# Performance work log

Hardware: AMD Instinct MI355X
Metric: run time of the kernel (lower is better)

Reference implementation:

```python
import jax, jax.numpy as jnp
import numpy as np

B, C_I, C_O, K, H, W = 8, 64, 64, 3, 256, 256
GROUPS = 16  # int(c_o / min(4, c_o)) = 64/4
EPS = 1e-5
PAD = K  # pad_x = pad_y = k + (bc-1) with bc_x=bc_y=1, k=3


def _conv(x, w):
    # x: (B, C_i, h, w), w: (C_o, C_i, K, K), valid conv, stride 1
    return jax.lax.conv_general_dilated(
        x, w, window_strides=(1, 1), padding='VALID',
        dimension_numbers=('NCHW', 'OIHW', 'NCHW'))


def setup_inputs() -> dict:
    key = jax.random.key(0)
    ks = jax.random.split(key, 10)
    s = 1.0 / np.sqrt(C_I * K * K)  # torch Conv2d default init bound
    wshape = (C_O, C_I, K, K)
    names = ['w_int', 'w_tl', 'w_tr', 'w_bl', 'w_br', 'w_top', 'w_bot', 'w_left', 'w_right']
    d = {'x': jax.random.normal(ks[0], (B, C_I, H, W), dtype=jnp.float32)}
    for i, n in enumerate(names):
        d[n] = jax.random.uniform(ks[i + 1], wshape, jnp.float32, -s, s)
    d['bias'] = jnp.zeros((1, C_O, 1, 1), jnp.float32)   # learnable_bias (init zeros)
    d['gamma'] = jnp.ones((C_O,), jnp.float32)           # GroupNorm weight
    d['beta'] = jnp.zeros((C_O,), jnp.float32)           # GroupNorm bias
    return d


def reference(x, w_int, w_tl, w_tr, w_bl, w_br, w_top, w_bot, w_left, w_right, bias, gamma, beta):
    p = PAD
    # corners -> (B,C,1,1)
    tl = _conv(x[:, :, :p, :p], w_tl)
    tr = _conv(x[:, :, :p, -p:], w_tr)
    bl = _conv(x[:, :, -p:, :p], w_bl)
    br = _conv(x[:, :, -p:, -p:], w_br)
    # edges -> (B,C,1,W-2) / (B,C,H-2,1)
    top = _conv(x[:, :, :p, :], w_top)
    bot = _conv(x[:, :, -p:, :], w_bot)
    left = _conv(x[:, :, :, :p], w_left)
    right = _conv(x[:, :, :, -p:], w_right)
    # interior -> (B,C,H-2,W-2)
    mid = _conv(x, w_int)
    mid = jnp.concatenate([left, mid, right], axis=3)       # (B,C,H-2,W)
    top_row = jnp.concatenate([tl, top, tr], axis=3)        # (B,C,1,W)
    bot_row = jnp.concatenate([bl, bot, br], axis=3)        # (B,C,1,W)
    # NOTE: original code puts the 'bottom' conv output first along dim 2
    y = jnp.concatenate([bot_row, mid, top_row], axis=2) + bias  # (B,C,H,W)
    # GroupNorm(16, 64)
    yg = y.reshape(B, GROUPS, -1)
    mu = jnp.mean(yg, axis=2, keepdims=True)
    var = jnp.var(yg, axis=2, keepdims=True)
    yn = ((yg - mu) * jax.lax.rsqrt(var + EPS)).reshape(B, C_O, H, W)
    yn = yn * gamma[None, :, None, None] + beta[None, :, None, None]
    # SELU activation; dropout(rate=0) is identity
    return jax.nn.selu(yn)
```

## Files before the change

kernel.cpp:

```cpp
#include <hip/hip_runtime.h>

#define B_ 8
#define CI 64
#define CO 64
#define H_ 256
#define W_ 256
#define EPS_ 1e-5f

#define SELU_SCALE 1.0507009873554805f
#define SELU_SA    1.7580993408473766f

typedef __attribute__((ext_vector_type(8))) short short8;
typedef __attribute__((ext_vector_type(4))) float f32x4;
typedef unsigned int u32;

__device__ __forceinline__ unsigned short f2bf(float f) {
    unsigned int u = __float_as_uint(f);
    u = (u + 0x7fffu + ((u >> 16) & 1u)) >> 16;
    return (unsigned short)u;
}
__device__ __forceinline__ float bf2f(unsigned short h) {
    return __uint_as_float(((unsigned)h) << 16);
}
__device__ __forceinline__ float selu_f(float u) {
    return (u > 0.f) ? SELU_SCALE * u : SELU_SA * (__expf(u) - 1.f);
}
__device__ __forceinline__ void gload_lds16(const void* g, void* l) {
    __builtin_amdgcn_global_load_lds(
        (const __attribute__((address_space(1))) u32*)g,
        (__attribute__((address_space(3))) u32*)l, 16, 0, 0);
}

__global__ __launch_bounds__(256) void prepass_fused(
    const float* __restrict__ x,
    const float* __restrict__ w_int,
    const float* __restrict__ w_bl, const float* __restrict__ w_br,
    const float* __restrict__ w_tl, const float* __restrict__ w_tr,
    const float* __restrict__ w_bot, const float* __restrict__ w_top,
    const float* __restrict__ w_left, const float* __restrict__ w_right,
    unsigned short* __restrict__ xpre,
    unsigned short* __restrict__ wpre9, float* __restrict__ wedge)
{
    __shared__ unsigned short ls[256 * 72];
    const int blk = blockIdx.x, t = threadIdx.x;

    if (blk < 2048) {
        const int row = blk & 255, b = blk >> 8;
        const int colq = t >> 2;
        const float* xb = x + ((size_t)(b * 64) * 256 + row) * 256;

        for (int sp = 0; sp < 4; ++sp) {
            const int cibase = sp * 16 + (t & 3) * 4;
            float4 v[4];
#pragma unroll
            for (int e = 0; e < 4; ++e)
                v[e] = *(const float4*)(xb + (size_t)(cibase + e) * 65536 + colq * 4);
#pragma unroll
            for (int jj = 0; jj < 4; ++jj) {
                const int col = colq * 4 + jj;
                const int sw  = (col & 7) << 3;
                ushort4 pk;
                pk.x = f2bf((&v[0].x)[jj]);
                pk.y = f2bf((&v[1].x)[jj]);
                pk.z = f2bf((&v[2].x)[jj]);
                pk.w = f2bf((&v[3].x)[jj]);
                *(ushort4*)&ls[col * 72 + (cibase ^ sw)] = pk;
            }
        }
        __syncthreads();
        unsigned short* xp = xpre + ((size_t)(b * 256 + row)) * 256 * 64;
        for (int q = 0; q < 8; ++q) {
            const int lin = q * 256 + t;
            const int col = lin >> 3, k = lin & 7;
            *(uint4*)(xp + col * 64 + k * 8) = *(const uint4*)&ls[col * 72 + k * 8];
        }
    } else {
        const int wb = blk - 2048;
        const int wid = wb / 9, pos = wb % 9;
        const float* src = (wid == 0) ? w_bl : (wid == 1) ? w_br
                         : (wid == 2) ? w_tl : (wid == 3) ? w_tr
                         : (wid == 4) ? w_bot : (wid == 5) ? w_top
                         : (wid == 6) ? w_left : (wid == 7) ? w_right : w_int;
        for (int k = 0; k < 16; ++k) {
            const int lin = k * 256 + t;
            const int co = lin >> 6, cip = lin & 63;
            const int ci = cip ^ ((co & 7) << 3);
            wpre9[(size_t)wid * 36864 + pos * 4096 + lin] =
                f2bf(src[(co * 64 + ci) * 9 + pos]);
            if (wid < 8) {
                const int c4 = lin >> 8, co2 = (lin >> 2) & 63, j = lin & 3;
                const int ci2 = c4 * 4 + j;
                wedge[(size_t)wid * 36864 + pos * 4096 + lin] =
                    src[(co2 * 64 + ci2) * 9 + pos];
            }
        }
    }
}

__global__ __launch_bounds__(512, 4) void conv_all(
    const unsigned short* __restrict__ xpre, const unsigned short* __restrict__ wpre9,
    const float* __restrict__ wedge, const float* __restrict__ bias,
    unsigned short* __restrict__ ybf, float* __restrict__ part)
{
    __shared__ unsigned short xs[10 * 40 * 64];
    __shared__ unsigned short wl3[3][4096];
    __shared__ float sred[8][16][2];
    const int t = threadIdx.x, w = t >> 6, lane = t & 63;
    const int b = blockIdx.z;
    const int l15 = lane & 15, lg = lane >> 4;
    const int sw15 = (l15 & 7) << 3;

    if (blockIdx.y < 32) {
        const unsigned short* wpre = wpre9 + 8 * 36864;
        const int r0 = blockIdx.y * 8, c0 = blockIdx.x * 32;

        for (int L = w; L < 50; L += 8) {
            const int j = L / 5, i = L % 5;
            int rr = r0 - 1 + j; rr = rr < 0 ? 0 : (rr > 255 ? 255 : rr);
            int col = c0 - 2 + i * 8 + (lane >> 3);
            col = col < 0 ? 0 : (col > 255 ? 255 : col);
            gload_lds16((const char*)xpre +
                            ((size_t)((b * 256 + rr) * 256 + col)) * 128 + (lane & 7) * 16,
                        (char*)xs + j * 5120 + i * 1024);
        }
        gload_lds16((const char*)wpre + 0 * 8192 + w * 1024 + lane * 16,
                    (char*)wl3[0] + w * 1024);
        gload_lds16((const char*)wpre + 1 * 8192 + w * 1024 + lane * 16,
                    (char*)wl3[1] + w * 1024);

        int jb[3];
#pragma unroll
        for (int kr = 0; kr < 3; ++kr) jb[kr] = (w + kr) * 5120;
        int offb[3][2][2];
#pragma unroll
        for (int kc = 0; kc < 3; ++kc)
#pragma unroll
            for (int n = 0; n < 2; ++n) {
                const int s = n * 16 + l15 + kc + 1;
#pragma unroll
                for (int ks = 0; ks < 2; ++ks) {
                    const int cib = ks * 32 + lg * 8;
                    offb[kc][n][ks] = s * 128 + ((cib ^ (((s + 6) & 7) << 3)) << 1);
                }
            }
        int afo[2][4];
#pragma unroll
        for (int ks = 0; ks < 2; ++ks)
#pragma unroll
            for (int m = 0; m < 4; ++m) {
                const int cib = ks * 32 + lg * 8;
                afo[ks][m] = (m * 16 + l15) * 128 + ((cib ^ sw15) << 1);
            }

        f32x4 acc[4][2];
#pragma unroll
        for (int m = 0; m < 4; ++m)
#pragma unroll
            for (int n = 0; n < 2; ++n)
                acc[m][n] = (f32x4){0.f, 0.f, 0.f, 0.f};

#pragma unroll
        for (int pos = 0; pos < 9; ++pos) {
            if (pos < 8) asm volatile("s_waitcnt vmcnt(1)" ::: "memory");
            else         asm volatile("s_waitcnt vmcnt(0)" ::: "memory");
            __builtin_amdgcn_s_barrier();
            __builtin_amdgcn_sched_barrier(0);
            if (pos + 2 <= 8)
                gload_lds16((const char*)wpre + (pos + 2) * 8192 + w * 1024 + lane * 16,
                            (char*)wl3[(pos + 2) % 3] + w * 1024);
            const int kr = pos / 3, kc = pos % 3;
            const char* wbuf = (const char*)wl3[pos % 3];
#pragma unroll
            for (int ks = 0; ks < 2; ++ks) {
                short8 bf[2], af[4];
#pragma unroll
                for (int n = 0; n < 2; ++n)
                    bf[n] = *(const short8*)((const char*)xs + jb[kr] + offb[kc][n][ks]);
#pragma unroll
                for (int m = 0; m < 4; ++m)
                    af[m] = *(const short8*)(wbuf + afo[ks][m]);
                __builtin_amdgcn_s_setprio(1);
#pragma unroll
                for (int m = 0; m < 4; ++m)
#pragma unroll
                    for (int n = 0; n < 2; ++n)
                        acc[m][n] = __builtin_amdgcn_mfma_f32_16x16x32_bf16(
                            af[m], bf[n], acc[m][n], 0, 0, 0);
                __builtin_amdgcn_s_setprio(0);
            }
        }

        const int r = r0 + w;
        const bool rmask = (r != 0) && (r != 255);
        float s4[4] = {0.f, 0.f, 0.f, 0.f}, q4[4] = {0.f, 0.f, 0.f, 0.f};
#pragma unroll
        for (int m = 0; m < 4; ++m)
#pragma unroll
            for (int n = 0; n < 2; ++n) {
                const int c = c0 + n * 16 + l15;
                const bool pmask = rmask && (c != 0) && (c != 255);
#pragma unroll
                for (int reg = 0; reg < 4; ++reg) {
                    const int co = m * 16 + lg * 4 + reg;
                    const float v = acc[m][n][reg] + bias[co];
                    if (pmask) {
                        ybf[(((size_t)b * 64 + co) * 256 + r) * 256 + c] = f2bf(v);
                        s4[m] += v; q4[m] += v * v;
                    }
                }
            }
#pragma unroll
        for (int off = 1; off < 16; off <<= 1)
#pragma unroll
            for (int m = 0; m < 4; ++m) {
                s4[m] += __shfl_xor(s4[m], off);
                q4[m] += __shfl_xor(q4[m], off);
            }
        if (l15 == 0) {
#pragma unroll
            for (int m = 0; m < 4; ++m) {
                sred[w][m * 4 + lg][0] = s4[m];
                sred[w][m * 4 + lg][1] = q4[m];
            }
        }
        __syncthreads();
        if (t < 32) {
            const int g = t & 15, sel = t >> 4;
            float v = 0.f;
#pragma unroll
            for (int ww = 0; ww < 8; ++ww) v += sred[ww][g][sel];
            const int slot = blockIdx.y * 8 + blockIdx.x;
            part[((size_t)(b * 512 + slot) * 16 + g) * 2 + sel] = v;
        }
        return;
    }

    const int job = (blockIdx.y - 32) * 8 + blockIdx.x;
    if (job > 24) return;

    if (job < 16) {
        const int edge = job >> 3, seg = job & 7;
        const int c0 = seg * 32;
        const char* wsrc = (const char*)wpre9 + (size_t)(4 + edge) * 73728;
        for (int L = w; L < 15; L += 8) {
            const int j = L / 5, i = L % 5;
            const int rr = (edge == 0) ? (253 + j) : j;
            int col = c0 - 2 + i * 8 + (lane >> 3);
            col = col < 0 ? 0 : (col > 255 ? 255 : col);
            gload_lds16((const char*)xpre +
                            ((size_t)((b * 256 + rr) * 256 + col)) * 128 + (lane & 7) * 16,
                        (char*)xs + j * 5120 + i * 1024);
        }
        gload_lds16(wsrc + 0 * 8192 + w * 1024 + lane * 16, (char*)wl3[0] + w * 1024);
        gload_lds16(wsrc + 1 * 8192 + w * 1024 + lane * 16, (char*)wl3[1] + w * 1024);

        const int cot = w & 3, nh = w >> 2;
        int offb2[3][2];
#pragma unroll
        for (int kc = 0; kc < 3; ++kc) {
            const int s = nh * 16 + l15 + kc + 1;
#pragma unroll
            for (int ks = 0; ks < 2; ++ks) {
                const int cib = ks * 32 + lg * 8;
                offb2[kc][ks] = s * 128 + ((cib ^ (((s + 6) & 7) << 3)) << 1);
            }
        }
        int afo2[2];
#pragma unroll
        for (int ks = 0; ks < 2; ++ks) {
            const int cib = ks * 32 + lg * 8;
            afo2[ks] = (cot * 16 + l15) * 128 + ((cib ^ sw15) << 1);
        }
        f32x4 acc0 = (f32x4){0.f, 0.f, 0.f, 0.f};

#pragma unroll
        for (int pos = 0; pos < 9; ++pos) {
            if (pos < 8) asm volatile("s_waitcnt vmcnt(1)" ::: "memory");
            else         asm volatile("s_waitcnt vmcnt(0)" ::: "memory");
            __builtin_amdgcn_s_barrier();
            __builtin_amdgcn_sched_barrier(0);
            if (pos + 2 <= 8)
                gload_lds16(wsrc + (pos + 2) * 8192 + w * 1024 + lane * 16,
                            (char*)wl3[(pos + 2) % 3] + w * 1024);
            const int kr = pos / 3, kc = pos % 3;
            const char* wbuf = (const char*)wl3[pos % 3];
#pragma unroll
            for (int ks = 0; ks < 2; ++ks) {
                const short8 bf = *(const short8*)((const char*)xs + kr * 5120 + offb2[kc][ks]);
                const short8 af = *(const short8*)(wbuf + afo2[ks]);
                acc0 = __builtin_amdgcn_mfma_f32_16x16x32_bf16(af, bf, acc0, 0, 0, 0);
            }
        }

        const int r_out = edge ? 255 : 0;
        const int c = c0 + nh * 16 + l15;
        const bool pmask = (c != 0) && (c != 255);
        float s = 0.f, q = 0.f;
#pragma unroll
        for (int reg = 0; reg < 4; ++reg) {
            const int co = cot * 16 + lg * 4 + reg;
            const float v = acc0[reg] + bias[co];
            if (pmask) {
                ybf[(((size_t)b * 64 + co) * 256 + r_out) * 256 + c] = f2bf(v);
                s += v; q += v * v;
            }
        }
        s += __shfl_xor(s, 1); q += __shfl_xor(q, 1);
        s += __shfl_xor(s, 2); q += __shfl_xor(q, 2);
        s += __shfl_xor(s, 4); q += __shfl_xor(q, 4);
        s += __shfl_xor(s, 8); q += __shfl_xor(q, 8);
        float* sb = (float*)sred;
        if (l15 == 0) { sb[(w * 4 + lg) * 2] = s; sb[(w * 4 + lg) * 2 + 1] = q; }
        __syncthreads();
        if (t < 32) {
            const int g = t & 15, sel = t >> 4;
            const int ct = g >> 2, sub = g & 3;
            const float v = sb[(ct * 4 + sub) * 2 + sel] + sb[((ct + 4) * 4 + sub) * 2 + sel];
            part[((size_t)(b * 512 + 256 + job) * 16 + g) * 2 + sel] = v;
        }
    } else if (job < 24) {
        const int jj = job - 16;
        const int edge = jj >> 2, seg = jj & 3;
        const int r0 = seg * 64;
        const int colbase = edge ? 253 : 0;
        unsigned short* xr = xs;
        for (int u = t; u < 1584; u += 512) {
            const int row = u / 24, rem = u % 24;
            const int cl = rem >> 3, sub = rem & 7;
            int rr = r0 - 1 + row; rr = rr < 0 ? 0 : (rr > 255 ? 255 : rr);
            const int col = colbase + cl;
            const uint4 v = *(const uint4*)(xpre +
                ((size_t)((b * 256 + rr) * 256 + col)) * 64 + sub * 8);
            *(uint4*)((char*)xr + row * 400 + cl * 128 + sub * 16) = v;
        }
        const char* wsrc = (const char*)wpre9 + (size_t)(6 + edge) * 73728;
        gload_lds16(wsrc + 0 * 8192 + w * 1024 + lane * 16, (char*)wl3[0] + w * 1024);
        gload_lds16(wsrc + 1 * 8192 + w * 1024 + lane * 16, (char*)wl3[1] + w * 1024);
        asm volatile("s_waitcnt lgkmcnt(0)" ::: "memory");

        const int cot = w & 3, np = w >> 2;
        int offlr[3][2];
#pragma unroll
        for (int kc = 0; kc < 3; ++kc) {
            const int key = (colbase + kc) & 7;
#pragma unroll
            for (int ks = 0; ks < 2; ++ks) {
                const int cib = ks * 32 + lg * 8;
                offlr[kc][ks] = kc * 128 + ((cib ^ (key << 3)) << 1);
            }
        }
        int rowb2[2];
#pragma unroll
        for (int j = 0; j < 2; ++j) rowb2[j] = ((np * 2 + j) * 16 + l15) * 400;
        int afo2[2];
#pragma unroll
        for (int ks = 0; ks < 2; ++ks) {
            const int cib = ks * 32 + lg * 8;
            afo2[ks] = (cot * 16 + l15) * 128 + ((cib ^ sw15) << 1);
        }
        f32x4 accA = (f32x4){0.f, 0.f, 0.f, 0.f};
        f32x4 accB = (f32x4){0.f, 0.f, 0.f, 0.f};

#pragma unroll
        for (int pos = 0; pos < 9; ++pos) {
            if (pos < 8) asm volatile("s_waitcnt vmcnt(1)" ::: "memory");
            else         asm volatile("s_waitcnt vmcnt(0)" ::: "memory");
            __builtin_amdgcn_s_barrier();
            __builtin_amdgcn_sched_barrier(0);
            if (pos + 2 <= 8)
                gload_lds16(wsrc + (pos + 2) * 8192 + w * 1024 + lane * 16,
                            (char*)wl3[(pos + 2) % 3] + w * 1024);
            const int kr = pos / 3, kc = pos % 3;
            const char* wbuf = (const char*)wl3[pos % 3];
#pragma unroll
            for (int ks = 0; ks < 2; ++ks) {
                const short8 af = *(const short8*)(wbuf + afo2[ks]);
                const short8 bfA = *(const short8*)((const char*)xr + rowb2[0] + kr * 400 + offlr[kc][ks]);
                const short8 bfB = *(const short8*)((const char*)xr + rowb2[1] + kr * 400 + offlr[kc][ks]);
                accA = __builtin_amdgcn_mfma_f32_16x16x32_bf16(af, bfA, accA, 0, 0, 0);
                accB = __builtin_amdgcn_mfma_f32_16x16x32_bf16(af, bfB, accB, 0, 0, 0);
            }
        }

        const int c_out = edge ? 255 : 0;
        float s = 0.f, q = 0.f;
#pragma unroll
        for (int j = 0; j < 2; ++j) {
            const int r = r0 + (np * 2 + j) * 16 + l15;
            const bool pmask = (r != 0) && (r != 255);
            const f32x4 a = j ? accB : accA;
#pragma unroll
            for (int reg = 0; reg < 4; ++reg) {
                const int co = cot * 16 + lg * 4 + reg;
                const float v = a[reg] + bias[co];
                if (pmask) {
                    ybf[(((size_t)b * 64 + co) * 256 + r) * 256 + c_out] = f2bf(v);
                    s += v; q += v * v;
                }
            }
        }
        s += __shfl_xor(s, 1); q += __shfl_xor(q, 1);
        s += __shfl_xor(s, 2); q += __shfl_xor(q, 2);
        s += __shfl_xor(s, 4); q += __shfl_xor(q, 4);
        s += __shfl_xor(s, 8); q += __shfl_xor(q, 8);
        float* sb = (float*)sred;
        if (l15 == 0) { sb[(w * 4 + lg) * 2] = s; sb[(w * 4 + lg) * 2 + 1] = q; }
        __syncthreads();
        if (t < 32) {
            const int g = t & 15, sel = t >> 4;
            const int ct = g >> 2, sub = g & 3;
            const float v = sb[(ct * 4 + sub) * 2 + sel] + sb[((ct + 4) * 4 + sub) * 2 + sel];
            part[((size_t)(b * 512 + 272 + jj) * 16 + g) * 2 + sel] = v;
        }
    } else {
        float* cred = (float*)sred;
        if (w < 4) {
            const int corner = w, co = lane;
            const int row0 = (corner < 2) ? 253 : 0;
            const int col0 = (corner & 1) ? 253 : 0;
            const int r_out = (corner < 2) ? 0 : 255;
            const int c_out = (corner & 1) ? 255 : 0;
            const float* wbase = wedge + (size_t)corner * 36864;
            float a0 = 0.f, a1 = 0.f, a2 = 0.f, a3 = 0.f;
#pragma unroll 1
            for (int pos = 0; pos < 9; ++pos) {
                const int kr = pos / 3, kc = pos % 3;
                const int row = row0 + kr, col = col0 + kc;
                const unsigned short* xp = xpre + ((size_t)((b * 256 + row) * 256 + col)) * 64;
                const int sw = (col & 7) << 3;
#pragma unroll
                for (int c4 = 0; c4 < 16; ++c4) {
                    const float4 wv = *(const float4*)(wbase + pos * 4096 + c4 * 256 + co * 4);
                    const ushort4 xv = *(const ushort4*)(xp + ((c4 * 4) ^ sw));
                    a0 = fmaf(wv.x, bf2f(xv.x), a0);
                    a1 = fmaf(wv.y, bf2f(xv.y), a1);
                    a2 = fmaf(wv.z, bf2f(xv.z), a2);
                    a3 = fmaf(wv.w, bf2f(xv.w), a3);
                }
            }
            const float v = (a0 + a1) + (a2 + a3) + bias[co];
            ybf[(((size_t)b * 64 + co) * 256 + r_out) * 256 + c_out] = f2bf(v);
            float s = v, q = v * v;
            s += __shfl_xor(s, 1); q += __shfl_xor(q, 1);
            s += __shfl_xor(s, 2); q += __shfl_xor(q, 2);
            if ((co & 3) == 0) {
                cred[(corner * 16 + (co >> 2)) * 2]     = s;
                cred[(corner * 16 + (co >> 2)) * 2 + 1] = q;
            }
        }
        __syncthreads();
        if (t < 32) {
            const int g = t & 15, sel = t >> 4;
            const float r = cred[(0 * 16 + g) * 2 + sel] + cred[(1 * 16 + g) * 2 + sel] +
                            cred[(2 * 16 + g) * 2 + sel] + cred[(3 * 16 + g) * 2 + sel];
            part[((size_t)(b * 512 + 280) * 16 + g) * 2 + sel] = r;
        }
    }
}

__global__ __launch_bounds__(256) void norm_bf2(
    const unsigned short* __restrict__ ybf, float* __restrict__ out,
    const float* __restrict__ part,
    const float* __restrict__ gamma, const float* __restrict__ beta)
{
    __shared__ float wred[4][2];
    __shared__ float mvs[2];
    const int t = threadIdx.x;
    const size_t e0 = (size_t)blockIdx.x * 2048;
    const int b  = (int)(e0 >> 22);
    const int ch = (int)((e0 >> 16) & 63);
    const int g  = ch >> 2;

    float s = 0.f, q = 0.f;
    for (int slot = t; slot < 281; slot += 256) {
        const size_t base = ((size_t)(b * 512 + slot) * 16 + g) * 2;
        s += part[base]; q += part[base + 1];
    }
#pragma unroll
    for (int off = 32; off; off >>= 1) {
        s += __shfl_down(s, off);
        q += __shfl_down(q, off);
    }
    if ((t & 63) == 0) { wred[t >> 6][0] = s; wred[t >> 6][1] = q; }
    __syncthreads();
    if (t == 0) {
        const float S = wred[0][0] + wred[1][0] + wred[2][0] + wred[3][0];
        const float Q = wred[0][1] + wred[1][1] + wred[2][1] + wred[3][1];
        const float inv_n = 1.0f / (4.0f * 65536.0f);
        const float mean = S * inv_n;
        const float var  = Q * inv_n - mean * mean;
        mvs[0] = mean;
        mvs[1] = rsqrtf(var + EPS_);
    }
    __syncthreads();
    const float mean = mvs[0], rstd = mvs[1];
    const float ga = gamma[ch] * rstd;
    const float be = beta[ch] - mean * ga;

    const size_t e = e0 + (size_t)t * 8;
    const uint4 v = *(const uint4*)(ybf + e);
    float f[8];
    f[0] = __uint_as_float(v.x << 16); f[1] = __uint_as_float(v.x & 0xffff0000u);
    f[2] = __uint_as_float(v.y << 16); f[3] = __uint_as_float(v.y & 0xffff0000u);
    f[4] = __uint_as_float(v.z << 16); f[5] = __uint_as_float(v.z & 0xffff0000u);
    f[6] = __uint_as_float(v.w << 16); f[7] = __uint_as_float(v.w & 0xffff0000u);
    float4 o0, o1;
    o0.x = selu_f(f[0] * ga + be); o0.y = selu_f(f[1] * ga + be);
    o0.z = selu_f(f[2] * ga + be); o0.w = selu_f(f[3] * ga + be);
    o1.x = selu_f(f[4] * ga + be); o1.y = selu_f(f[5] * ga + be);
    o1.z = selu_f(f[6] * ga + be); o1.w = selu_f(f[7] * ga + be);
    *(float4*)(out + e)     = o0;
    *(float4*)(out + e + 4) = o1;
}

__global__ __launch_bounds__(256) void conv_main(
    const float* __restrict__ x, const float* __restrict__ w,
    const float* __restrict__ bias, float* __restrict__ y)
{
    const int c = threadIdx.x;
    const int r = blockIdx.x;
    const int b = blockIdx.y;
    const int rr = (r == 0) ? (H_ - 3) : ((r == H_ - 1) ? 0 : (r - 1));
    const int cc = min(max(c - 1, 0), W_ - 3);
    float acc[CO];
#pragma unroll
    for (int co = 0; co < CO; ++co) acc[co] = 0.f;
    const float* xb = x + (size_t)b * CI * H_ * W_;
    for (int ci = 0; ci < CI; ++ci) {
        const float* xp = xb + ((size_t)ci * H_ + rr) * W_ + cc;
        float xv[9];
#pragma unroll
        for (int kr = 0; kr < 3; ++kr)
#pragma unroll
            for (int kc = 0; kc < 3; ++kc)
                xv[kr * 3 + kc] = xp[kr * W_ + kc];
        const float* wci = w + ci * 9;
#pragma unroll
        for (int co = 0; co < CO; ++co) {
            const float* wp = wci + co * (CI * 9);
            float a = acc[co];
#pragma unroll
            for (int k = 0; k < 9; ++k) a = fmaf(xv[k], wp[k], a);
            acc[co] = a;
        }
    }
#pragma unroll
    for (int co = 0; co < CO; ++co)
        y[(((size_t)b * CO + co) * H_ + r) * W_ + c] = acc[co] + bias[co];
}

__global__ __launch_bounds__(256) void conv_edge(
    const float* __restrict__ x,
    const float* __restrict__ w_bot, const float* __restrict__ w_top,
    const float* __restrict__ w_left, const float* __restrict__ w_right,
    const float* __restrict__ bias, float* __restrict__ y)
{
    const int b     = blockIdx.x;
    const int edge  = blockIdx.y;
    const int seg   = blockIdx.z;
    const int el    = threadIdx.x & 63;
    const int chunk = threadIdx.x >> 6;
    const int e     = seg * 64 + el;
    const bool active = (e < 254);
    const int ec    = active ? e : 253;
    const float* w = (edge == 0) ? w_bot : (edge == 1) ? w_top
                   : (edge == 2) ? w_left : w_right;
    int r_out, c_out, rr, cc;
    if (edge == 0)      { r_out = 0;      c_out = 1 + ec; rr = H_ - 3; cc = ec; }
    else if (edge == 1) { r_out = H_ - 1; c_out = 1 + ec; rr = 0;      cc = ec; }
    else if (edge == 2) { r_out = 1 + ec; c_out = 0;      rr = ec;     cc = 0; }
    else                { r_out = 1 + ec; c_out = W_ - 1; rr = ec;     cc = W_ - 3; }
    float acc[CO];
#pragma unroll
    for (int co = 0; co < CO; ++co) acc[co] = 0.f;
    const float* xb = x + (size_t)b * CI * H_ * W_;
    const int ci0 = chunk * 16;
    for (int ci = ci0; ci < ci0 + 16; ++ci) {
        const float* xp = xb + ((size_t)ci * H_ + rr) * W_ + cc;
        float xv[9];
#pragma unroll
        for (int kr = 0; kr < 3; ++kr)
#pragma unroll
            for (int kc = 0; kc < 3; ++kc)
                xv[kr * 3 + kc] = xp[kr * W_ + kc];
#pragma unroll
        for (int co = 0; co < CO; ++co) {
            const float* wp = w + co * (CI * 9) + ci * 9;
            float a = acc[co];
#pragma unroll
            for (int k = 0; k < 9; ++k) a = fmaf(xv[k], wp[k], a);
            acc[co] = a;
        }
    }
    __shared__ float lds[64][65];
    for (int s = 0; s < 4; ++s) {
        if (chunk == s) {
            if (s == 0) {
#pragma unroll
                for (int co = 0; co < CO; ++co) lds[el][co] = acc[co];
            } else {
#pragma unroll
                for (int co = 0; co < CO; ++co) lds[el][co] += acc[co];
            }
        }
        __syncthreads();
    }
    if (chunk == 0 && active) {
#pragma unroll
        for (int co = 0; co < CO; ++co)
            y[(((size_t)b * CO + co) * H_ + r_out) * W_ + c_out] = lds[el][co] + bias[co];
    }
}

__global__ __launch_bounds__(256) void conv_corner(
    const float* __restrict__ x,
    const float* __restrict__ w_bl, const float* __restrict__ w_br,
    const float* __restrict__ w_tl, const float* __restrict__ w_tr,
    const float* __restrict__ bias, float* __restrict__ y)
{
    const int b      = blockIdx.x;
    const int corner = threadIdx.x >> 6;
    const int co     = threadIdx.x & 63;
    const float* w = (corner == 0) ? w_bl : (corner == 1) ? w_br
                   : (corner == 2) ? w_tl : w_tr;
    const int rr    = (corner < 2) ? (H_ - 3) : 0;
    const int cc    = (corner & 1) ? (W_ - 3) : 0;
    const int r_out = (corner < 2) ? 0 : (H_ - 1);
    const int c_out = (corner & 1) ? (W_ - 1) : 0;
    const float* xb = x + (size_t)b * CI * H_ * W_;
    float a = 0.f;
    for (int ci = 0; ci < CI; ++ci) {
        const float* xp = xb + ((size_t)ci * H_ + rr) * W_ + cc;
        const float* wp = w + ((size_t)co * CI + ci) * 9;
#pragma unroll
        for (int kr = 0; kr < 3; ++kr)
#pragma unroll
            for (int kc = 0; kc < 3; ++kc)
                a = fmaf(xp[kr * W_ + kc], wp[kr * 3 + kc], a);
    }
    y[(((size_t)b * CO + co) * H_ + r_out) * W_ + c_out] = a + bias[co];
}

__global__ __launch_bounds__(256) void stats_kernel(
    const float* __restrict__ y, float* __restrict__ ws)
{
    const int bid   = blockIdx.x;
    const int chunk = bid & 3;
    const int g     = (bid >> 2) & 15;
    const int b     = bid >> 6;
    const float* p  = y + ((size_t)(b * 64 + g * 4 + chunk)) * (H_ * W_);
    float s = 0.f, q = 0.f;
    for (int i = threadIdx.x; i < (H_ * W_ / 4); i += 256) {
        float4 v = reinterpret_cast<const float4*>(p)[i];
        s += v.x + v.y + v.z + v.w;
        q += v.x * v.x + v.y * v.y + v.z * v.z + v.w * v.w;
    }
#pragma unroll
    for (int off = 32; off; off >>= 1) {
        s += __shfl_down(s, off);
        q += __shfl_down(q, off);
    }
    __shared__ float red[8];
    const int wid = threadIdx.x >> 6;
    if ((threadIdx.x & 63) == 0) { red[wid * 2] = s; red[wid * 2 + 1] = q; }
    __syncthreads();
    if (threadIdx.x == 0) {
        ws[bid * 2]     = red[0] + red[2] + red[4] + red[6];
        ws[bid * 2 + 1] = red[1] + red[3] + red[5] + red[7];
    }
}

__global__ __launch_bounds__(256) void norm_stats(
    float* __restrict__ y, const float* __restrict__ st,
    const float* __restrict__ gamma, const float* __restrict__ beta)
{
    const size_t t = (size_t)blockIdx.x * 256 + threadIdx.x;
    const size_t e = t * 4;
    const int b  = (int)(e >> 22);
    const int ch = (int)((e >> 16) & 63);
    const int g  = ch >> 2;
    const int sb = ((b * 16 + g) * 4) * 2;
    const float S = st[sb] + st[sb + 2] + st[sb + 4] + st[sb + 6];
    const float Q = st[sb + 1] + st[sb + 3] + st[sb + 5] + st[sb + 7];
    const float inv_n = 1.0f / (4.0f * H_ * W_);
    const float mean  = S * inv_n;
    const float var   = Q * inv_n - mean * mean;
    const float rstd  = rsqrtf(var + EPS_);
    const float ga = gamma[ch] * rstd;
    const float be = beta[ch] - mean * ga;
    float4 v = reinterpret_cast<float4*>(y)[t];
    float u;
    u = v.x * ga + be; v.x = selu_f(u);
    u = v.y * ga + be; v.y = selu_f(u);
    u = v.z * ga + be; v.z = selu_f(u);
    u = v.w * ga + be; v.w = selu_f(u);
    reinterpret_cast<float4*>(y)[t] = v;
}

extern "C" void kernel_launch(void* const* d_in, const int* in_sizes, int n_in,
                              void* d_out, int out_size, void* d_ws, size_t ws_size,
                              hipStream_t stream) {
    const float* x       = (const float*)d_in[0];
    const float* w_int   = (const float*)d_in[1];
    const float* w_tl    = (const float*)d_in[2];
    const float* w_tr    = (const float*)d_in[3];
    const float* w_bl    = (const float*)d_in[4];
    const float* w_br    = (const float*)d_in[5];
    const float* w_top   = (const float*)d_in[6];
    const float* w_bot   = (const float*)d_in[7];
    const float* w_left  = (const float*)d_in[8];
    const float* w_right = (const float*)d_in[9];
    const float* bias    = (const float*)d_in[10];
    const float* gamma   = (const float*)d_in[11];
    const float* beta    = (const float*)d_in[12];

    float* out = (float*)d_out;

    const size_t XPRE  = 67108864ull;
    const size_t YBF   = 67108864ull;
    const size_t WPRE9 = 663552ull;
    const size_t WEDGE = 1179648ull;
    const size_t PART  = 524288ull;
    const size_t NEED  = XPRE + YBF + WPRE9 + WEDGE + PART;

    if (ws_size >= NEED) {
        char* base = (char*)d_ws;
        unsigned short* xpre  = (unsigned short*)base;  base += XPRE;
        unsigned short* ybf   = (unsigned short*)base;  base += YBF;
        unsigned short* wpre9 = (unsigned short*)base;  base += WPRE9;
        float*          wedge = (float*)base;           base += WEDGE;
        float*          part  = (float*)base;

        prepass_fused<<<dim3(2129), 256, 0, stream>>>(
            x, w_int, w_bl, w_br, w_tl, w_tr, w_bot, w_top, w_left, w_right,
            xpre, wpre9, wedge);
        conv_all<<<dim3(8, 36, 8), 512, 0, stream>>>(
            xpre, wpre9, wedge, bias, ybf, part);
        norm_bf2<<<dim3(16384), 256, 0, stream>>>(ybf, out, part, gamma, beta);
    } else {
        float* stats = (float*)d_ws;
        conv_main<<<dim3(H_, B_), 256, 0, stream>>>(x, w_int, bias, out);
        conv_edge<<<dim3(B_, 4, 4), 256, 0, stream>>>(x, w_bot, w_top, w_left, w_right, bias, out);
        conv_corner<<<dim3(B_), 256, 0, stream>>>(x, w_bl, w_br, w_tl, w_tr, bias, out);
        stats_kernel<<<dim3(512), 256, 0, stream>>>(out, stats);
        norm_stats<<<dim3(32768), 256, 0, stream>>>(out, stats, gamma, beta);
    }
}
```

Before: 168.5 us.

## Keep interior conv weights in registers, remap warps to row-group by co-tile

The interior conv path no longer streams weights through a triple-buffered LDS ring with per-tap barriers. Each warp now owns one 16-channel output tile and four rows, and loads all nine taps of its weight fragment straight from global memory into registers. The LDS weight buffer is removed and the edge paths reuse spare space in the x tile instead, which lowers LDS usage so the launch bound can target 6 blocks per CU. The cost is many more VGPRs for the weight fragments (18 short8 values), which could cause spills at the tighter launch bound, plus global loads of weights from every warp.

```diff
diff --git a/kernel.cpp b/kernel.cpp
--- a/kernel.cpp
+++ b/kernel.cpp
@@ -97,13 +97,12 @@
     }
 }
 
-__global__ __launch_bounds__(512, 4) void conv_all(
+__global__ __launch_bounds__(512, 6) void conv_all(
     const unsigned short* __restrict__ xpre, const unsigned short* __restrict__ wpre9,
     const float* __restrict__ wedge, const float* __restrict__ bias,
     unsigned short* __restrict__ ybf, float* __restrict__ part)
 {
     __shared__ unsigned short xs[10 * 40 * 64];
-    __shared__ unsigned short wl3[3][4096];
     __shared__ float sred[8][16][2];
     const int t = threadIdx.x, w = t >> 6, lane = t & 63;
     const int b = blockIdx.z;
@@ -111,8 +110,19 @@
     const int sw15 = (l15 & 7) << 3;
 
     if (blockIdx.y < 32) {
-        const unsigned short* wpre = wpre9 + 8 * 36864;
+        const unsigned short* wint = wpre9 + 8 * 36864;
         const int r0 = blockIdx.y * 8, c0 = blockIdx.x * 32;
+        const int rg = w >> 2, ct = w & 3;
+
+        short8 af[9][2];
+#pragma unroll
+        for (int pos = 0; pos < 9; ++pos)
+#pragma unroll
+            for (int ks = 0; ks < 2; ++ks) {
+                const int cib = ks * 32 + lg * 8;
+                af[pos][ks] = *(const short8*)((const char*)wint + pos * 8192 +
+                                  (ct * 16 + l15) * 128 + ((cib ^ sw15) << 1));
+            }
 
         for (int L = w; L < 50; L += 8) {
             const int j = L / 5, i = L % 5;
@@ -123,14 +133,7 @@
                             ((size_t)((b * 256 + rr) * 256 + col)) * 128 + (lane & 7) * 16,
                         (char*)xs + j * 5120 + i * 1024);
         }
-        gload_lds16((const char*)wpre + 0 * 8192 + w * 1024 + lane * 16,
-                    (char*)wl3[0] + w * 1024);
-        gload_lds16((const char*)wpre + 1 * 8192 + w * 1024 + lane * 16,
-                    (char*)wl3[1] + w * 1024);
-
-        int jb[3];
-#pragma unroll
-        for (int kr = 0; kr < 3; ++kr) jb[kr] = (w + kr) * 5120;
+
         int offb[3][2][2];
 #pragma unroll
         for (int kc = 0; kc < 3; ++kc)
@@ -143,92 +146,70 @@
                     offb[kc][n][ks] = s * 128 + ((cib ^ (((s + 6) & 7) << 3)) << 1);
                 }
             }
-        int afo[2][4];
-#pragma unroll
-        for (int ks = 0; ks < 2; ++ks)
-#pragma unroll
-            for (int m = 0; m < 4; ++m) {
-                const int cib = ks * 32 + lg * 8;
-                afo[ks][m] = (m * 16 + l15) * 128 + ((cib ^ sw15) << 1);
-            }
+        int rbase[4];
+#pragma unroll
+        for (int jr = 0; jr < 4; ++jr) rbase[jr] = (rg * 4 + jr) * 5120;
 
         f32x4 acc[4][2];
 #pragma unroll
-        for (int m = 0; m < 4; ++m)
+        for (int jr = 0; jr < 4; ++jr)
 #pragma unroll
             for (int n = 0; n < 2; ++n)
-                acc[m][n] = (f32x4){0.f, 0.f, 0.f, 0.f};
+                acc[jr][n] = (f32x4){0.f, 0.f, 0.f, 0.f};
+
+        __syncthreads();
 
 #pragma unroll
         for (int pos = 0; pos < 9; ++pos) {
-            if (pos < 8) asm volatile("s_waitcnt vmcnt(1)" ::: "memory");
-            else         asm volatile("s_waitcnt vmcnt(0)" ::: "memory");
-            __builtin_amdgcn_s_barrier();
-            __builtin_amdgcn_sched_barrier(0);
-            if (pos + 2 <= 8)
-                gload_lds16((const char*)wpre + (pos + 2) * 8192 + w * 1024 + lane * 16,
-                            (char*)wl3[(pos + 2) % 3] + w * 1024);
             const int kr = pos / 3, kc = pos % 3;
-            const char* wbuf = (const char*)wl3[pos % 3];
 #pragma unroll
             for (int ks = 0; ks < 2; ++ks) {
-                short8 bf[2], af[4];
-#pragma unroll
-                for (int n = 0; n < 2; ++n)
-                    bf[n] = *(const short8*)((const char*)xs + jb[kr] + offb[kc][n][ks]);
-#pragma unroll
-                for (int m = 0; m < 4; ++m)
-                    af[m] = *(const short8*)(wbuf + afo[ks][m]);
-                __builtin_amdgcn_s_setprio(1);
-#pragma unroll
-                for (int m = 0; m < 4; ++m)
+                short8 bf[4][2];
+#pragma unroll
+                for (int jr = 0; jr < 4; ++jr)
 #pragma unroll
                     for (int n = 0; n < 2; ++n)
-                        acc[m][n] = __builtin_amdgcn_mfma_f32_16x16x32_bf16(
-                            af[m], bf[n], acc[m][n], 0, 0, 0);
-                __builtin_amdgcn_s_setprio(0);
-            }
-        }
-
-        const int r = r0 + w;
-        const bool rmask = (r != 0) && (r != 255);
-        float s4[4] = {0.f, 0.f, 0.f, 0.f}, q4[4] = {0.f, 0.f, 0.f, 0.f};
-#pragma unroll
-        for (int m = 0; m < 4; ++m)
+                        bf[jr][n] = *(const short8*)((const char*)xs +
+                                        rbase[jr] + kr * 5120 + offb[kc][n][ks]);
+#pragma unroll
+                for (int jr = 0; jr < 4; ++jr)
+#pragma unroll
+                    for (int n = 0; n < 2; ++n)
+                        acc[jr][n] = __builtin_amdgcn_mfma_f32_16x16x32_bf16(
+                            af[pos][ks], bf[jr][n], acc[jr][n], 0, 0, 0);
+            }
+        }
+
+        float s = 0.f, q = 0.f;
+#pragma unroll
+        for (int jr = 0; jr < 4; ++jr) {
+            const int r = r0 + rg * 4 + jr;
+            const bool rmask = (r != 0) && (r != 255);
 #pragma unroll
             for (int n = 0; n < 2; ++n) {
                 const int c = c0 + n * 16 + l15;
                 const bool pmask = rmask && (c != 0) && (c != 255);
 #pragma unroll
                 for (int reg = 0; reg < 4; ++reg) {
-                    const int co = m * 16 + lg * 4 + reg;
-                    const float v = acc[m][n][reg] + bias[co];
+                    const int co = ct * 16 + lg * 4 + reg;
+                    const float v = acc[jr][n][reg] + bias[co];
                     if (pmask) {
                         ybf[(((size_t)b * 64 + co) * 256 + r) * 256 + c] = f2bf(v);
-                        s4[m] += v; q4[m] += v * v;
+                        s += v; q += v * v;
                     }
                 }
             }
-#pragma unroll
-        for (int off = 1; off < 16; off <<= 1)
-#pragma unroll
-            for (int m = 0; m < 4; ++m) {
-                s4[m] += __shfl_xor(s4[m], off);
-                q4[m] += __shfl_xor(q4[m], off);
-            }
-        if (l15 == 0) {
-#pragma unroll
-            for (int m = 0; m < 4; ++m) {
-                sred[w][m * 4 + lg][0] = s4[m];
-                sred[w][m * 4 + lg][1] = q4[m];
-            }
-        }
+        }
+        s += __shfl_xor(s, 1); q += __shfl_xor(q, 1);
+        s += __shfl_xor(s, 2); q += __shfl_xor(q, 2);
+        s += __shfl_xor(s, 4); q += __shfl_xor(q, 4);
+        s += __shfl_xor(s, 8); q += __shfl_xor(q, 8);
+        if (l15 == 0) { sred[w][lg][0] = s; sred[w][lg][1] = q; }
         __syncthreads();
         if (t < 32) {
             const int g = t & 15, sel = t >> 4;
-            float v = 0.f;
-#pragma unroll
-            for (int ww = 0; ww < 8; ++ww) v += sred[ww][g][sel];
+            const int gct = g >> 2, glg = g & 3;
+            const float v = sred[gct][glg][sel] + sred[gct + 4][glg][sel];
             const int slot = blockIdx.y * 8 + blockIdx.x;
             part[((size_t)(b * 512 + slot) * 16 + g) * 2 + sel] = v;
         }
@@ -237,6 +218,7 @@
 
     const int job = (blockIdx.y - 32) * 8 + blockIdx.x;
     if (job > 24) return;
+    char* wl3b = (char*)xs + 26624;
 
     if (job < 16) {
         const int edge = job >> 3, seg = job & 7;
@@ -251,8 +233,8 @@
                             ((size_t)((b * 256 + rr) * 256 + col)) * 128 + (lane & 7) * 16,
                         (char*)xs + j * 5120 + i * 1024);
         }
-        gload_lds16(wsrc + 0 * 8192 + w * 1024 + lane * 16, (char*)wl3[0] + w * 1024);
-        gload_lds16(wsrc + 1 * 8192 + w * 1024 + lane * 16, (char*)wl3[1] + w * 1024);
+        gload_lds16(wsrc + 0 * 8192 + w * 1024 + lane * 16, wl3b + 0 * 8192 + w * 1024);
+        gload_lds16(wsrc + 1 * 8192 + w * 1024 + lane * 16, wl3b + 1 * 8192 + w * 1024);
 
         const int cot = w & 3, nh = w >> 2;
         int offb2[3][2];
@@ -281,9 +263,9 @@
             __builtin_amdgcn_sched_barrier(0);
             if (pos + 2 <= 8)
                 gload_lds16(wsrc + (pos + 2) * 8192 + w * 1024 + lane * 16,
-                            (char*)wl3[(pos + 2) % 3] + w * 1024);
+                            wl3b + ((pos + 2) % 3) * 8192 + w * 1024);
             const int kr = pos / 3, kc = pos % 3;
-            const char* wbuf = (const char*)wl3[pos % 3];
+            const char* wbuf = wl3b + (pos % 3) * 8192;
 #pragma unroll
             for (int ks = 0; ks < 2; ++ks) {
                 const short8 bf = *(const short8*)((const char*)xs + kr * 5120 + offb2[kc][ks]);
@@ -314,8 +296,8 @@
         __syncthreads();
         if (t < 32) {
             const int g = t & 15, sel = t >> 4;
-            const int ct = g >> 2, sub = g & 3;
-            const float v = sb[(ct * 4 + sub) * 2 + sel] + sb[((ct + 4) * 4 + sub) * 2 + sel];
+            const int gct = g >> 2, sub = g & 3;
+            const float v = sb[(gct * 4 + sub) * 2 + sel] + sb[((gct + 4) * 4 + sub) * 2 + sel];
             part[((size_t)(b * 512 + 256 + job) * 16 + g) * 2 + sel] = v;
         }
     } else if (job < 24) {
@@ -334,8 +316,8 @@
             *(uint4*)((char*)xr + row * 400 + cl * 128 + sub * 16) = v;
         }
         const char* wsrc = (const char*)wpre9 + (size_t)(6 + edge) * 73728;
-        gload_lds16(wsrc + 0 * 8192 + w * 1024 + lane * 16, (char*)wl3[0] + w * 1024);
-        gload_lds16(wsrc + 1 * 8192 + w * 1024 + lane * 16, (char*)wl3[1] + w * 1024);
+        gload_lds16(wsrc + 0 * 8192 + w * 1024 + lane * 16, wl3b + 0 * 8192 + w * 1024);
+        gload_lds16(wsrc + 1 * 8192 + w * 1024 + lane * 16, wl3b + 1 * 8192 + w * 1024);
         asm volatile("s_waitcnt lgkmcnt(0)" ::: "memory");
 
         const int cot = w & 3, np = w >> 2;
@@ -369,9 +351,9 @@
             __builtin_amdgcn_sched_barrier(0);
             if (pos + 2 <= 8)
                 gload_lds16(wsrc + (pos + 2) * 8192 + w * 1024 + lane * 16,
-                            (char*)wl3[(pos + 2) % 3] + w * 1024);
+                            wl3b + ((pos + 2) % 3) * 8192 + w * 1024);
             const int kr = pos / 3, kc = pos % 3;
-            const char* wbuf = (const char*)wl3[pos % 3];
+            const char* wbuf = wl3b + (pos % 3) * 8192;
 #pragma unroll
             for (int ks = 0; ks < 2; ++ks) {
                 const short8 af = *(const short8*)(wbuf + afo2[ks]);
@@ -408,8 +390,8 @@
         __syncthreads();
         if (t < 32) {
             const int g = t & 15, sel = t >> 4;
-            const int ct = g >> 2, sub = g & 3;
-            const float v = sb[(ct * 4 + sub) * 2 + sel] + sb[((ct + 4) * 4 + sub) * 2 + sel];
+            const int gct = g >> 2, sub = g & 3;
+            const float v = sb[(gct * 4 + sub) * 2 + sel] + sb[((gct + 4) * 4 + sub) * 2 + sel];
             part[((size_t)(b * 512 + 272 + jj) * 16 + g) * 2 + sel] = v;
         }
     } else {
```

New measurement: 559.9 us. 3.32x slower.
